# Kernel optimization log

Hardware: AMD Instinct MI355X
Metric: run time of the kernel (lower is better)

Reference implementation:

```python
import jax, jax.numpy as jnp
import numpy as np

B, N, F_IN, HID, NHEADS, NCLASS = 256, 200, 768, 32, 8, 2
ALPHA = 0.3          # LeakyReLU negative slope
NEG_INF = -9e15      # mask value used by the torch code for fp32
BN_EPS = 1e-5


def setup_inputs() -> dict:
    key = jax.random.key(0)
    ks = jax.random.split(key, 12)
    xav = lambda k, shape: jax.random.uniform(
        k, shape, jnp.float32, -1.0, 1.0) * 1.414 * np.sqrt(6.0 / (shape[0] + shape[-1]))
    return {
        "feat_matrix": jax.random.normal(ks[0], (B, N, F_IN), jnp.float32),
        "adj": jax.random.randint(ks[1], (B, N, N), 0, 2, jnp.int32),
        # 8 attention heads: W [H, 768, 32], a [H, 64, 1]
        "Wh": xav(ks[2], (NHEADS, F_IN, HID)),
        "ah": xav(ks[3], (NHEADS, 2 * HID, 1)),
        # output GAT layers over concatenated 256-dim features
        "W_sent": xav(ks[4], (HID * NHEADS, NCLASS)),
        "a_sent": xav(ks[5], (2 * NCLASS, 1)),
        "W_para": xav(ks[6], (HID * NHEADS, NCLASS)),
        "a_para": xav(ks[7], (2 * NCLASS, 1)),
        "W_qt": xav(ks[8], (HID * NHEADS, HID)),
        "a_qt": xav(ks[9], (2 * HID, 1)),
        "W2": xav(ks[10], (HID, 2)),
        # BatchNorm1d(nodes_num=200) params/buffers (eval mode)
        "bn_gamma": jnp.ones((N,), jnp.float32),
        "bn_beta": jnp.zeros((N,), jnp.float32),
        "bn_mean": jnp.zeros((N,), jnp.float32),
        "bn_var": jnp.ones((N,), jnp.float32),
    }


def gat_layer(x, mask, W, a, concat):
    # x: [B,N,Fin], W: [Fin,Fout], a: [2*Fout,1]
    h = x @ W                                   # [B,N,Fout]
    fo = W.shape[1]
    s1 = h @ a[:fo, 0]                          # [B,N]  (h_i . a1)
    s2 = h @ a[fo:, 0]                          # [B,N]  (h_j . a2)
    e = jax.nn.leaky_relu(s1[:, :, None] + s2[:, None, :], ALPHA)  # [B,N,N]
    att = jax.nn.softmax(jnp.where(mask, e, NEG_INF), axis=-1)
    out = att @ h                               # [B,N,Fout]
    return jax.nn.elu(out) if concat else out


def reference(feat_matrix, adj, Wh, ah, W_sent, a_sent, W_para, a_para,
              W_qt, a_qt, W2, bn_gamma, bn_beta, bn_mean, bn_var):
    mask = adj > 0                              # [B,N,N]
    # 8 heads, concat -> [B,N,256]
    heads = jax.vmap(lambda W, a: gat_layer(feat_matrix, mask, W, a, True))(Wh, ah)
    x = jnp.transpose(heads, (1, 2, 0, 3)).reshape(B, N, NHEADS * HID)
    # BatchNorm1d over node axis (channels = N), eval mode
    inv = bn_gamma / jnp.sqrt(bn_var + BN_EPS)
    x = (x - bn_mean[None, :, None]) * inv[None, :, None] + bn_beta[None, :, None]
    logits_sent = jax.nn.sigmoid(gat_layer(x, mask, W_sent, a_sent, False))   # [B,N,2]
    logits_para = jax.nn.elu(gat_layer(x, mask, W_para, a_para, False))       # [B,N,2]
    h_qt = gat_layer(x, mask, W_qt, a_qt, False)[:, 0, :]                     # [B,32]
    logits_qtype = jax.nn.elu(h_qt @ W2).reshape(-1, 2)                       # [B,2]
    return logits_sent, logits_para, logits_qtype
```

## Files before the change

### kernel.cpp

```cpp
#include <hip/hip_runtime.h>
#include <hip/hip_bf16.h>

#define ALPHA   0.3f
#define NEG_INF (-9e15f)
#define BN_EPS  1e-5f

typedef _Float16 f16x4 __attribute__((ext_vector_type(4)));
typedef _Float16 f16x8 __attribute__((ext_vector_type(8)));
typedef float    f32x4 __attribute__((ext_vector_type(4)));
typedef unsigned u32x4 __attribute__((ext_vector_type(4)));
typedef unsigned long long u64;

__global__ __launch_bounds__(256) void k_wcat(const float* __restrict__ Wh,
                                              _Float16* __restrict__ WT)
{
    const int o = blockIdx.x * 256 + threadIdx.x;
    const int n = o / 768, k = o - n * 768;
    WT[o] = (_Float16)Wh[((n >> 5) * 768 + k) * 32 + (n & 31)];
}

__global__ __launch_bounds__(256) void k_pack(const int* __restrict__ adj,
                                              u64* __restrict__ Mw)
{
    const int w = threadIdx.x >> 6, lane = threadIdx.x & 63;
    const int row = blockIdx.x * 4 + w;
    const int* ar = adj + (size_t)row * 200;
    #pragma unroll
    for (int t = 0; t < 4; ++t) {
        const int j = t * 64 + lane;
        const int a = ar[j < 200 ? j : 199];
        const u64 bal = __ballot(j < 200 && a > 0);
        if (lane == 0) Mw[(size_t)row * 4 + t] = bal;
    }
}

__global__ __launch_bounds__(256) void k_gemm1(const float* __restrict__ A,
                                               const _Float16* __restrict__ WT,
                                               float* __restrict__ H)
{
    __shared__ _Float16 Af[64][72];
    __shared__ _Float16 Bf[256][72];
    const int tid  = threadIdx.x;
    const int wv   = tid >> 6;
    const int lane = tid & 63;
    const int r16  = lane & 15, q = lane >> 4;
    const size_t m_blk = (size_t)blockIdx.x * 64;
    const int wn = wv * 64;
    const int arow = tid >> 2, akb = (tid & 3) * 16;
    f32x4 acc[4][4] = {};

    for (int kt = 0; kt < 768; kt += 64) {
        __syncthreads();
        #pragma unroll
        for (int p = 0; p < 4; ++p) {
            const float4 a4 = *(const float4*)&A[(m_blk + arow) * 768 + kt + akb + p * 4];
            f16x4 h4 = { (_Float16)a4.x, (_Float16)a4.y, (_Float16)a4.z, (_Float16)a4.w };
            *(f16x4*)&Af[arow][akb + p * 4] = h4;
        }
        #pragma unroll
        for (int p = 0; p < 8; ++p) {
            f16x8 w8 = *(const f16x8*)&WT[tid * 768 + kt + p * 8];
            *(f16x8*)&Bf[tid][p * 8] = w8;
        }
        __syncthreads();
        #pragma unroll
        for (int kc = 0; kc < 64; kc += 32) {
            f16x8 af[4], bf[4];
            #pragma unroll
            for (int i = 0; i < 4; ++i)
                af[i] = *(const f16x8*)&Af[i * 16 + r16][kc + q * 8];
            #pragma unroll
            for (int j = 0; j < 4; ++j)
                bf[j] = *(const f16x8*)&Bf[wn + j * 16 + r16][kc + q * 8];
            #pragma unroll
            for (int i = 0; i < 4; ++i)
                #pragma unroll
                for (int j = 0; j < 4; ++j)
                    acc[i][j] = __builtin_amdgcn_mfma_f32_16x16x32_f16(
                        af[i], bf[j], acc[i][j], 0, 0, 0);
        }
    }
    #pragma unroll
    for (int i = 0; i < 4; ++i)
        #pragma unroll
        for (int j = 0; j < 4; ++j)
            #pragma unroll
            for (int r = 0; r < 4; ++r) {
                const int m = i * 16 + q * 4 + r;
                const int n = wn + j * 16 + r16;
                H[(m_blk + m) * 256 + n] = acc[i][j][r];
            }
}

__global__ __launch_bounds__(256, 4) void k_attn1(float* __restrict__ H,
    const unsigned* __restrict__ Mw, const float* __restrict__ ah,
    const float* __restrict__ bng, const float* __restrict__ bnb,
    const float* __restrict__ bnm, const float* __restrict__ bnv)
{
    __shared__ alignas(16) _Float16 HsT[32][232];
    __shared__ alignas(16) unsigned Ml[208][8];
    __shared__ alignas(16) float s2[224];
    __shared__ float s1[208];
    __shared__ float av[64];
    __shared__ float bnA[208], bnB[208];
    const int tid  = threadIdx.x;
    const int b    = blockIdx.x >> 3;
    const int head = blockIdx.x & 7;
    float* Hb = H + (size_t)b * 200 * 256 + head * 32;
    const unsigned* Mb = Mw + (size_t)b * 200 * 8;

    for (int idx = tid; idx < 6400; idx += 256) {
        int n = idx >> 5, f = idx & 31;
        HsT[f][n] = (_Float16)Hb[n * 256 + f];
    }
    for (int idx = tid; idx < 32 * 32; idx += 256) {
        int f = idx >> 5, c = 200 + (idx & 31);
        HsT[f][c] = (_Float16)0.f;
    }
    for (int idx = tid; idx < 208 * 8; idx += 256) {
        int rr = idx >> 3, wd = idx & 7;
        Ml[rr][wd] = (rr < 200) ? Mb[rr * 8 + wd] : 0u;
    }
    if (tid < 64) av[tid] = ah[head * 64 + tid];
    if (tid < 208) {
        float iv = 0.f, cb = 0.f;
        if (tid < 200) {
            iv = bng[tid] * rsqrtf(bnv[tid] + BN_EPS);
            cb = bnb[tid] - bnm[tid] * iv;
        }
        bnA[tid] = iv; bnB[tid] = cb;
    }
    __syncthreads();

    if (tid < 200) {
        float v1 = 0.f, v2 = 0.f;
        #pragma unroll
        for (int f = 0; f < 32; f += 4) {
            const float4 h4 = *(const float4*)&Hb[tid * 256 + f];
            v1 += h4.x * av[f]      + h4.y * av[f + 1]
                + h4.z * av[f + 2]  + h4.w * av[f + 3];
            v2 += h4.x * av[32 + f]     + h4.y * av[32 + f + 1]
                + h4.z * av[32 + f + 2] + h4.w * av[32 + f + 3];
        }
        s1[tid] = v1; s2[tid] = v2;
    } else {
        if (tid < 208) s1[tid] = 0.f;
        if (tid < 224) s2[tid] = 0.f;
    }
    __syncthreads();

    const int lane = tid & 63, wv = tid >> 6;
    const int r16 = lane & 15, q = lane >> 4;

    for (int tile = wv; tile < 13; tile += 4) {
        const int m0  = tile * 16;
        const int row = m0 + r16;
        const float s1i = s1[row];
        const u32x4 mwa = *(const u32x4*)&Ml[row][0];
        const u32x4 mwb = *(const u32x4*)&Ml[row][4];
        const unsigned mw[7] = {mwa[0], mwa[1], mwa[2], mwa[3],
                                mwb[0], mwb[1], mwb[2]};

        float m = -INFINITY;
        #pragma unroll
        for (int ks = 0; ks < 7; ++ks) {
            const f32x4 sA = *(const f32x4*)&s2[ks * 32 + q * 8];
            const f32x4 sB = *(const f32x4*)&s2[ks * 32 + q * 8 + 4];
            const unsigned wb = mw[ks] >> (q * 8);
            #pragma unroll
            for (int e = 0; e < 8; ++e) {
                const float sv = (e < 4) ? sA[e] : sB[e - 4];
                const float t = s1i + sv;
                const float tl = fmaxf(t, ALPHA * t);
                m = fmaxf(m, ((wb >> e) & 1u) ? tl : -INFINITY);
            }
        }
        m = fmaxf(m, __shfl_xor(m, 16));
        m = fmaxf(m, __shfl_xor(m, 32));

        float s = 0.f;
        f16x8 pa[7];
        #pragma unroll
        for (int ks = 0; ks < 7; ++ks) {
            const f32x4 sA = *(const f32x4*)&s2[ks * 32 + q * 8];
            const f32x4 sB = *(const f32x4*)&s2[ks * 32 + q * 8 + 4];
            const unsigned wb = mw[ks] >> (q * 8);
            #pragma unroll
            for (int e = 0; e < 8; ++e) {
                const float sv = (e < 4) ? sA[e] : sB[e - 4];
                float t = s1i + sv;
                t = fmaxf(t, ALPHA * t);
                float pe = __expf(t - m);
                pe = ((wb >> e) & 1u) ? pe : 0.f;
                s += pe;
                pa[ks][e] = (_Float16)pe;
            }
        }
        s += __shfl_xor(s, 16);
        s += __shfl_xor(s, 32);
        const float sinv = 1.f / s;

        f32x4 acc0 = {0.f, 0.f, 0.f, 0.f}, acc1 = {0.f, 0.f, 0.f, 0.f};
        #pragma unroll
        for (int ks = 0; ks < 7; ++ks) {
            const int k0 = ks * 32 + q * 8;
            const f16x8 b0 = *(const f16x8*)&HsT[r16][k0];
            const f16x8 b1 = *(const f16x8*)&HsT[16 + r16][k0];
            acc0 = __builtin_amdgcn_mfma_f32_16x16x32_f16(pa[ks], b0, acc0, 0, 0, 0);
            acc1 = __builtin_amdgcn_mfma_f32_16x16x32_f16(pa[ks], b1, acc1, 0, 0, 0);
        }
        float rv[4];
        #pragma unroll
        for (int r = 0; r < 4; ++r) rv[r] = __shfl(sinv, q * 4 + r);
        #pragma unroll
        for (int r = 0; r < 4; ++r) {
            const int i = m0 + q * 4 + r;
            if (i < 200) {
                float o0 = acc0[r] * rv[r];
                float o1 = acc1[r] * rv[r];
                o0 = o0 > 0.f ? o0 : expm1f(o0);
                o1 = o1 > 0.f ? o1 : expm1f(o1);
                const float ga = bnA[i], gb = bnB[i];
                Hb[i * 256 + r16]      = o0 * ga + gb;
                Hb[i * 256 + 16 + r16] = o1 * ga + gb;
            }
        }
    }
}

__global__ __launch_bounds__(256) void k_gemm2(const float* __restrict__ X,
    const float* __restrict__ Ws, const float* __restrict__ Wp,
    const float* __restrict__ Wq, float* __restrict__ Y)
{
    __shared__ float Wl[256][48];
    __shared__ float XsT[64][68];
    const int tid = threadIdx.x;
    {
        const int k = tid;
        #pragma unroll
        for (int c = 0; c < 36; ++c) {
            float v;
            if      (c == 0) v = Ws[k * 2 + 0];
            else if (c == 1) v = Ws[k * 2 + 1];
            else if (c == 2) v = Wp[k * 2 + 0];
            else if (c == 3) v = Wp[k * 2 + 1];
            else             v = Wq[k * 32 + (c - 4)];
            Wl[k][12 * (c / 9) + (c % 9)] = v;
        }
    }
    const int r  = tid & 63;
    const int cg = tid >> 6;
    const size_t row0 = (size_t)blockIdx.x * 64;
    float acc[9] = {};

    for (int kt = 0; kt < 256; kt += 64) {
        __syncthreads();
        #pragma unroll
        for (int i = 0; i < 4; ++i) {
            int l = tid + 256 * i;
            int row = l >> 4;
            int k4 = (l & 15) * 4;
            const float4 x4 = *(const float4*)&X[(row0 + row) * 256 + kt + k4];
            XsT[k4 + 0][row] = x4.x; XsT[k4 + 1][row] = x4.y;
            XsT[k4 + 2][row] = x4.z; XsT[k4 + 3][row] = x4.w;
        }
        __syncthreads();
        #pragma unroll 4
        for (int k = 0; k < 64; ++k) {
            const float xv = XsT[k][r];
            const float4 w0 = *(const float4*)&Wl[kt + k][12 * cg + 0];
            const float4 w1 = *(const float4*)&Wl[kt + k][12 * cg + 4];
            const float  w2 = Wl[kt + k][12 * cg + 8];
            acc[0] += xv * w0.x; acc[1] += xv * w0.y;
            acc[2] += xv * w0.z; acc[3] += xv * w0.w;
            acc[4] += xv * w1.x; acc[5] += xv * w1.y;
            acc[6] += xv * w1.z; acc[7] += xv * w1.w;
            acc[8] += xv * w2;
        }
    }
    float* yr = Y + (row0 + r) * 36 + cg * 9;
    #pragma unroll
    for (int c = 0; c < 9; ++c) yr[c] = acc[c];
}

__global__ __launch_bounds__(256) void k_attn2(const float* __restrict__ Y,
    const int* __restrict__ adj, const float* __restrict__ a_s,
    const float* __restrict__ a_p, const float* __restrict__ a_q,
    const float* __restrict__ W2, float* __restrict__ out)
{
    __shared__ float Ys[200][37];
    __shared__ float s1s[200], s2s[200], p1s[200], p2s[200], sq2[200];
    __shared__ float p0[200];
    __shared__ float hqt[32];
    __shared__ float sumq_s;
    __shared__ float asl[4], apl[4], aql[64], w2l[64];
    const int tid  = threadIdx.x;
    const int b    = blockIdx.x >> 1;
    const int half = blockIdx.x & 1;
    const float* Yb = Y + (size_t)b * 7200;
    const int* adjb = adj + (size_t)b * 200 * 200;

    for (int idx = tid; idx < 7200; idx += 256) {
        int j = idx / 36;
        int c = idx - j * 36;
        Ys[j][c] = Yb[idx];
    }
    if (tid < 4)  { asl[tid] = a_s[tid]; apl[tid] = a_p[tid]; }
    if (tid < 64) { aql[tid] = a_q[tid]; w2l[tid] = W2[tid]; }
    __syncthreads();

    if (tid < 200) {
        int j = tid;
        s1s[j] = Ys[j][0] * asl[0] + Ys[j][1] * asl[1];
        s2s[j] = Ys[j][0] * asl[2] + Ys[j][1] * asl[3];
        p1s[j] = Ys[j][2] * apl[0] + Ys[j][3] * apl[1];
        p2s[j] = Ys[j][2] * apl[2] + Ys[j][3] * apl[3];
        float a = 0.f;
        #pragma unroll
        for (int f = 0; f < 32; ++f) a += Ys[j][4 + f] * aql[32 + f];
        sq2[j] = a;
    }
    __syncthreads();

    const int w = tid >> 6, lane = tid & 63;
    for (int ii = w; ii < 100; ii += 4) {
        const int i = half * 100 + ii;
        const float s1i = s1s[i], p1i = p1s[i];
        float ms = -INFINITY, mp = -INFINITY;
        float es[4], ep[4];
        #pragma unroll
        for (int t = 0; t < 4; ++t) {
            int j = lane + 64 * t;
            int jj = j < 200 ? j : 0;
            int a = (j < 200) ? adjb[i * 200 + j] : 0;
            float e1 = s1i + s2s[jj]; e1 = e1 >= 0.f ? e1 : ALPHA * e1;
            float e2 = p1i + p2s[jj]; e2 = e2 >= 0.f ? e2 : ALPHA * e2;
            es[t] = (a > 0) ? e1 : (j < 200 ? NEG_INF : -INFINITY);
            ep[t] = (a > 0) ? e2 : (j < 200 ? NEG_INF : -INFINITY);
            ms = fmaxf(ms, es[t]); mp = fmaxf(mp, ep[t]);
        }
        #pragma unroll
        for (int off = 32; off >= 1; off >>= 1) {
            ms = fmaxf(ms, __shfl_xor(ms, off));
            mp = fmaxf(mp, __shfl_xor(mp, off));
        }
        float ss = 0.f, sp = 0.f, os0 = 0.f, os1 = 0.f, op0 = 0.f, op1 = 0.f;
        #pragma unroll
        for (int t = 0; t < 4; ++t) {
            int j = lane + 64 * t;
            int jj = j < 200 ? j : 0;
            float pes = __expf(es[t] - ms);
            float pep = __expf(ep[t] - mp);
            ss += pes; sp += pep;
            os0 += pes * Ys[jj][0]; os1 += pes * Ys[jj][1];
            op0 += pep * Ys[jj][2]; op1 += pep * Ys[jj][3];
        }
        #pragma unroll
        for (int off = 32; off >= 1; off >>= 1) {
            ss  += __shfl_xor(ss, off);  sp  += __shfl_xor(sp, off);
            os0 += __shfl_xor(os0, off); os1 += __shfl_xor(os1, off);
            op0 += __shfl_xor(op0, off); op1 += __shfl_xor(op1, off);
        }
        if (lane == 0) {
            float v0 = os0 / ss, v1 = os1 / ss;
            out[((size_t)b * 200 + i) * 2 + 0] = 1.f / (1.f + __expf(-v0));
            out[((size_t)b * 200 + i) * 2 + 1] = 1.f / (1.f + __expf(-v1));
            float q0 = op0 / sp, q1 = op1 / sp;
            out[102400 + ((size_t)b * 200 + i) * 2 + 0] = q0 > 0.f ? q0 : expm1f(q0);
            out[102400 + ((size_t)b * 200 + i) * 2 + 1] = q1 > 0.f ? q1 : expm1f(q1);
        }
    }

    if (half == 0 && tid < 64) {
        float s1q = 0.f;
        #pragma unroll
        for (int f = 0; f < 32; ++f) s1q += Ys[0][4 + f] * aql[f];
        float mq = -INFINITY;
        float eq[4];
        #pragma unroll
        for (int t = 0; t < 4; ++t) {
            int j = tid + 64 * t;
            int jj = j < 200 ? j : 0;
            int a = (j < 200) ? adjb[j] : 0;
            float e = s1q + sq2[jj]; e = e >= 0.f ? e : ALPHA * e;
            eq[t] = (a > 0) ? e : (j < 200 ? NEG_INF : -INFINITY);
            mq = fmaxf(mq, eq[t]);
        }
        #pragma unroll
        for (int off = 32; off >= 1; off >>= 1) mq = fmaxf(mq, __shfl_xor(mq, off));
        float sq = 0.f;
        #pragma unroll
        for (int t = 0; t < 4; ++t) {
            int j = tid + 64 * t;
            float pe = __expf(eq[t] - mq);
            sq += pe;
            if (j < 200) p0[j] = pe;
        }
        #pragma unroll
        for (int off = 32; off >= 1; off >>= 1) sq += __shfl_xor(sq, off);
        if (tid == 0) sumq_s = sq;
    }
    __syncthreads();
    if (half == 0 && tid < 32) {
        float acc = 0.f;
        for (int j = 0; j < 200; ++j) acc += p0[j] * Ys[j][4 + tid];
        hqt[tid] = acc / sumq_s;
    }
    __syncthreads();
    if (half == 0 && tid < 2) {
        float v = 0.f;
        #pragma unroll
        for (int f = 0; f < 32; ++f) v += hqt[f] * w2l[f * 2 + tid];
        out[204800 + (size_t)b * 2 + tid] = v > 0.f ? v : expm1f(v);
    }
}

extern "C" void kernel_launch(void* const* d_in, const int* in_sizes, int n_in,
                              void* d_out, int out_size, void* d_ws, size_t ws_size,
                              hipStream_t stream) {
    const float* feat   = (const float*)d_in[0];
    const int*   adj    = (const int*)  d_in[1];
    const float* Wh     = (const float*)d_in[2];
    const float* ah     = (const float*)d_in[3];
    const float* W_sent = (const float*)d_in[4];
    const float* a_sent = (const float*)d_in[5];
    const float* W_para = (const float*)d_in[6];
    const float* a_para = (const float*)d_in[7];
    const float* W_qt   = (const float*)d_in[8];
    const float* a_qt   = (const float*)d_in[9];
    const float* W2     = (const float*)d_in[10];
    const float* bng    = (const float*)d_in[11];
    const float* bnb    = (const float*)d_in[12];
    const float* bnm    = (const float*)d_in[13];
    const float* bnv    = (const float*)d_in[14];

    float* H = (float*)d_ws;
    float* Y = H + (size_t)51200 * 256;
    _Float16* WT = (_Float16*)(Y + (size_t)51200 * 36);
    u64* Mw = (u64*)Y;
    float* out = (float*)d_out;

    k_wcat<<<768, 256, 0, stream>>>(Wh, WT);
    k_pack<<<12800, 256, 0, stream>>>(adj, Mw);
    k_gemm1<<<800, 256, 0, stream>>>(feat, WT, H);
    k_attn1<<<2048, 256, 0, stream>>>(H, (const unsigned*)Mw, ah, bng, bnb, bnm, bnv);
    k_gemm2<<<800, 256, 0, stream>>>(H, W_sent, W_para, W_qt, Y);
    k_attn2<<<512, 256, 0, stream>>>(Y, adj, a_sent, a_para, a_qt, W2, out);
}
```

Measured before the change: 562.7 us.

## Fuse weight transpose into adjacency pack and double attention block width

The weight-cast kernel is folded into the adjacency bit-pack kernel, which removes one launch. Both attention kernels move from 256 to 512 threads per block. In k_attn1 the prologue is split across thread groups: one group transposes H into shared memory while another computes the attention scores and batch-norm coefficients and a third loads the mask words. This overlaps the setup phases and removes a barrier. The trade-off is that k_attn1 has only 13 row tiles for 8 waves, so some waves idle in the main loop, and the larger blocks may lower occupancy.

```diff
diff --git a/kernel.cpp b/kernel.cpp
--- a/kernel.cpp
+++ b/kernel.cpp
@@ -11,17 +11,16 @@
 typedef unsigned u32x4 __attribute__((ext_vector_type(4)));
 typedef unsigned long long u64;
 
-__global__ __launch_bounds__(256) void k_wcat(const float* __restrict__ Wh,
+__global__ __launch_bounds__(256) void k_pack(const int* __restrict__ adj,
+                                              u64* __restrict__ Mw,
+                                              const float* __restrict__ Wh,
                                               _Float16* __restrict__ WT)
 {
-    const int o = blockIdx.x * 256 + threadIdx.x;
-    const int n = o / 768, k = o - n * 768;
-    WT[o] = (_Float16)Wh[((n >> 5) * 768 + k) * 32 + (n & 31)];
-}
-
-__global__ __launch_bounds__(256) void k_pack(const int* __restrict__ adj,
-                                              u64* __restrict__ Mw)
-{
+    if (blockIdx.x < 768) {
+        const int o = blockIdx.x * 256 + threadIdx.x;
+        const int n = o / 768, k = o - n * 768;
+        WT[o] = (_Float16)Wh[((n >> 5) * 768 + k) * 32 + (n & 31)];
+    }
     const int w = threadIdx.x >> 6, lane = threadIdx.x & 63;
     const int row = blockIdx.x * 4 + w;
     const int* ar = adj + (size_t)row * 200;
@@ -92,7 +91,7 @@
             }
 }
 
-__global__ __launch_bounds__(256, 4) void k_attn1(float* __restrict__ H,
+__global__ __launch_bounds__(512, 4) void k_attn1(float* __restrict__ H,
     const unsigned* __restrict__ Mw, const float* __restrict__ ah,
     const float* __restrict__ bng, const float* __restrict__ bnb,
     const float* __restrict__ bnm, const float* __restrict__ bnv)
@@ -100,8 +99,7 @@
     __shared__ alignas(16) _Float16 HsT[32][232];
     __shared__ alignas(16) unsigned Ml[208][8];
     __shared__ alignas(16) float s2[224];
-    __shared__ float s1[208];
-    __shared__ float av[64];
+    __shared__ alignas(16) float s1[208];
     __shared__ float bnA[208], bnB[208];
     const int tid  = threadIdx.x;
     const int b    = blockIdx.x >> 3;
@@ -109,50 +107,47 @@
     float* Hb = H + (size_t)b * 200 * 256 + head * 32;
     const unsigned* Mb = Mw + (size_t)b * 200 * 8;
 
-    for (int idx = tid; idx < 6400; idx += 256) {
-        int n = idx >> 5, f = idx & 31;
-        HsT[f][n] = (_Float16)Hb[n * 256 + f];
-    }
-    for (int idx = tid; idx < 32 * 32; idx += 256) {
-        int f = idx >> 5, c = 200 + (idx & 31);
-        HsT[f][c] = (_Float16)0.f;
-    }
-    for (int idx = tid; idx < 208 * 8; idx += 256) {
-        int rr = idx >> 3, wd = idx & 7;
-        Ml[rr][wd] = (rr < 200) ? Mb[rr * 8 + wd] : 0u;
-    }
-    if (tid < 64) av[tid] = ah[head * 64 + tid];
-    if (tid < 208) {
-        float iv = 0.f, cb = 0.f;
-        if (tid < 200) {
-            iv = bng[tid] * rsqrtf(bnv[tid] + BN_EPS);
-            cb = bnb[tid] - bnm[tid] * iv;
-        }
-        bnA[tid] = iv; bnB[tid] = cb;
-    }
-    __syncthreads();
-
-    if (tid < 200) {
+    if (tid < 256) {
+        for (int idx = tid; idx < 6400; idx += 256) {
+            int n = idx >> 5, f = idx & 31;
+            HsT[f][n] = (_Float16)Hb[n * 256 + f];
+        }
+        for (int idx = tid; idx < 32 * 32; idx += 256) {
+            int f = idx >> 5, c = 200 + (idx & 31);
+            HsT[f][c] = (_Float16)0.f;
+        }
+    } else if (tid < 456) {
+        const int row = tid - 256;
+        const float* avg = ah + head * 64;
         float v1 = 0.f, v2 = 0.f;
         #pragma unroll
         for (int f = 0; f < 32; f += 4) {
-            const float4 h4 = *(const float4*)&Hb[tid * 256 + f];
-            v1 += h4.x * av[f]      + h4.y * av[f + 1]
-                + h4.z * av[f + 2]  + h4.w * av[f + 3];
-            v2 += h4.x * av[32 + f]     + h4.y * av[32 + f + 1]
-                + h4.z * av[32 + f + 2] + h4.w * av[32 + f + 3];
-        }
-        s1[tid] = v1; s2[tid] = v2;
+            const float4 h4 = *(const float4*)&Hb[row * 256 + f];
+            const float4 a1 = *(const float4*)&avg[f];
+            const float4 a2 = *(const float4*)&avg[32 + f];
+            v1 += h4.x * a1.x + h4.y * a1.y + h4.z * a1.z + h4.w * a1.w;
+            v2 += h4.x * a2.x + h4.y * a2.y + h4.z * a2.z + h4.w * a2.w;
+        }
+        s1[row] = v1; s2[row] = v2;
+        const float iv = bng[row] * rsqrtf(bnv[row] + BN_EPS);
+        bnA[row] = iv; bnB[row] = bnb[row] - bnm[row] * iv;
     } else {
-        if (tid < 208) s1[tid] = 0.f;
-        if (tid < 224) s2[tid] = 0.f;
+        const int t2 = tid - 456;
+        for (int idx = t2; idx < 416; idx += 56) {
+            const int rr = idx >> 1, hf = idx & 1;
+            u32x4 mv = {0u, 0u, 0u, 0u};
+            if (rr < 200) mv = *(const u32x4*)&Mb[rr * 8 + hf * 4];
+            *(u32x4*)&Ml[rr][hf * 4] = mv;
+        }
+        if (t2 < 8)  s1[200 + t2] = 0.f;
+        if (t2 >= 8 && t2 < 32) s2[200 + (t2 - 8)] = 0.f;
     }
     __syncthreads();
 
     const int lane = tid & 63, wv = tid >> 6;
     const int r16 = lane & 15, q = lane >> 4;
 
-    for (int tile = wv; tile < 13; tile += 4) {
+    for (int tile = wv; tile < 13; tile += 8) {
         const int m0  = tile * 16;
         const int row = m0 + r16;
         const float s1i = s1[row];
@@ -283,7 +278,7 @@
     for (int c = 0; c < 9; ++c) yr[c] = acc[c];
 }
 
-__global__ __launch_bounds__(256) void k_attn2(const float* __restrict__ Y,
+__global__ __launch_bounds__(512, 4) void k_attn2(const float* __restrict__ Y,
     const int* __restrict__ adj, const float* __restrict__ a_s,
     const float* __restrict__ a_p, const float* __restrict__ a_q,
     const float* __restrict__ W2, float* __restrict__ out)
@@ -300,13 +295,13 @@
     const float* Yb = Y + (size_t)b * 7200;
     const int* adjb = adj + (size_t)b * 200 * 200;
 
-    for (int idx = tid; idx < 7200; idx += 256) {
+    for (int idx = tid; idx < 7200; idx += 512) {
         int j = idx / 36;
         int c = idx - j * 36;
         Ys[j][c] = Yb[idx];
     }
     if (tid < 4)  { asl[tid] = a_s[tid]; apl[tid] = a_p[tid]; }
-    if (tid < 64) { aql[tid] = a_q[tid]; w2l[tid] = W2[tid]; }
+    if (tid >= 64 && tid < 128) { aql[tid - 64] = a_q[tid - 64]; w2l[tid - 64] = W2[tid - 64]; }
     __syncthreads();
 
     if (tid < 200) {
@@ -323,7 +318,7 @@
     __syncthreads();
 
     const int w = tid >> 6, lane = tid & 63;
-    for (int ii = w; ii < 100; ii += 4) {
+    for (int ii = w; ii < 100; ii += 8) {
         const int i = half * 100 + ii;
         const float s1i = s1s[i], p1i = p1s[i];
         float ms = -INFINITY, mp = -INFINITY;
@@ -440,10 +435,9 @@
     u64* Mw = (u64*)Y;
     float* out = (float*)d_out;
 
-    k_wcat<<<768, 256, 0, stream>>>(Wh, WT);
-    k_pack<<<12800, 256, 0, stream>>>(adj, Mw);
+    k_pack<<<12800, 256, 0, stream>>>(adj, Mw, Wh, WT);
     k_gemm1<<<800, 256, 0, stream>>>(feat, WT, H);
-    k_attn1<<<2048, 256, 0, stream>>>(H, (const unsigned*)Mw, ah, bng, bnb, bnm, bnv);
+    k_attn1<<<2048, 512, 0, stream>>>(H, (const unsigned*)Mw, ah, bng, bnb, bnm, bnv);
     k_gemm2<<<800, 256, 0, stream>>>(H, W_sent, W_para, W_qt, Y);
-    k_attn2<<<512, 256, 0, stream>>>(Y, adj, a_sent, a_para, a_qt, W2, out);
-}
+    k_attn2<<<512, 512, 0, stream>>>(Y, adj, a_sent, a_para, a_qt, W2, out);
+}
```

Measured after the change: 566.8 us. Within noise of the previous version (+0.7%).
